# Kernel tuning notes

Measured on AMD Instinct MI355X. Metric: run time of the kernel, lower is better.

Reference implementation:

```python
import jax, jax.numpy as jnp
import numpy as np
from jax import lax

B, T, NX, NY = 4, 5, 512, 512
HID = 64
N_FP = 4
INV_R = 1000.0


def _build_Q():
    # 7-point space-time Laplacian stencil on the (t, y, x) grid, matching
    # torch.permute(x[i], (0, 2, 1)).flatten() ordering (t outer, y, x inner).
    idx = np.arange(T * NY * NX, dtype=np.int32).reshape(T, NY, NX)
    rows = [idx.ravel()]
    cols = [idx.ravel()]
    vals = [np.full(idx.size, 6.01, np.float32)]  # diag: 6 neighbors + kappa^2

    def add(a, b):
        rows.append(a.ravel()); cols.append(b.ravel())
        vals.append(np.full(a.size, -1.0, np.float32))
        rows.append(b.ravel()); cols.append(a.ravel())
        vals.append(np.full(a.size, -1.0, np.float32))

    add(idx[:-1], idx[1:])          # t neighbors
    add(idx[:, :-1], idx[:, 1:])    # y neighbors
    add(idx[:, :, :-1], idx[:, :, 1:])  # x neighbors
    return (np.concatenate(rows), np.concatenate(cols), np.concatenate(vals))


def setup_inputs() -> dict:
    key = jax.random.key(0)
    ks = jax.random.split(key, 7)
    gt = jax.random.normal(ks[0], (B, T, NX, NY), jnp.float32)
    x = jax.random.normal(ks[1], (B, T, NX, NY), jnp.float32)
    yobs = jax.random.normal(ks[2], (B, T, NX, NY), jnp.float32)
    mask = jax.random.randint(ks[3], (B, T, NX, NY), 0, 2).astype(jnp.int32)
    W1 = jax.random.normal(ks[4], (HID, T, 3, 3), jnp.float32) * 0.05
    b1 = jnp.zeros((HID,), jnp.float32)
    W2 = jax.random.normal(ks[5], (T, HID, 3, 3), jnp.float32) * 0.05
    b2 = jnp.zeros((T,), jnp.float32)
    qr, qc, qv = _build_Q()
    return {"gt": gt, "x": x, "yobs": yobs, "mask": mask,
            "W1": W1, "b1": b1, "W2": W2, "b2": b2,
            "Q_rows": jnp.asarray(qr), "Q_cols": jnp.asarray(qc),
            "Q_vals": jnp.asarray(qv), "n_fp": N_FP}


def _phi_r(x, W1, b1, W2, b2):
    dn = ("NCHW", "OIHW", "NCHW")
    h = lax.conv_general_dilated(x, W1, (1, 1), "SAME", dimension_numbers=dn)
    h = jax.nn.relu(h + b1[None, :, None, None])
    o = lax.conv_general_dilated(h, W2, (1, 1), "SAME", dimension_numbers=dn)
    return o + b2[None, :, None, None]


def _var_cost_row(gt, x, yobs, maskf, Q_rows, Q_cols, Q_vals):
    # dy term: inv_R = 1000*I restricted to observed entries
    dy = (x - yobs) * maskf                       # model_H
    dy_term = INV_R * jnp.sum(maskf * dy * dy, axis=(1, 2, 3))  # [B]
    # x^T Q x on the permuted/flattened field (sparse COO quadratic form)
    xp = jnp.transpose(x, (0, 1, 3, 2)).reshape(x.shape[0], -1)  # [B, T*NY*NX]
    xtQx = jnp.einsum("bn,n,bn->b", xp[:, Q_rows], Q_vals, xp[:, Q_cols])
    loss_OI = dy_term + xtQx
    # weighted MSE with w = ones(5) == plain per-batch MSE
    loss_mse = jnp.mean((gt - x) ** 2, axis=(1, 2, 3))
    return jnp.stack([loss_mse, loss_OI], axis=1)  # [B, 2]


def reference(gt, x, yobs, mask, W1, b1, W2, b2, Q_rows, Q_cols, Q_vals, n_fp):
    maskf = mask.astype(x.dtype)
    unmeas = 1.0 - maskf
    y_obs = yobs * maskf
    x_k = x
    rows = []
    for _ in range(n_fp):
        rows.append(_var_cost_row(gt, x_k, yobs, maskf, Q_rows, Q_cols, Q_vals))
        x_k = _phi_r(x_k, W1, b1, W2, b2) * unmeas + y_obs  # fixed-point step
    x_k = _phi_r(x_k, W1, b1, W2, b2)
    rows.append(_var_cost_row(gt, x_k, yobs, maskf, Q_rows, Q_cols, Q_vals))
    cmp_loss = jnp.stack(rows, axis=1)  # [B, n_fp+1, 2]
    return x_k, cmp_loss
```

## Files before the change

kernel.cpp:

```cpp
#include <hip/hip_runtime.h>
#include <hip/hip_bf16.h>

#define NXD 512
#define NYD 512
#define TD 5
#define BD 4
#define HIDD 64
#define PLANE (NXD*NYD)
#define VOL (TD*PLANE)
#define CBLK 1024

typedef __bf16 bf16x8 __attribute__((ext_vector_type(8)));
typedef __bf16 bf16x4 __attribute__((ext_vector_type(4)));
typedef float  f32x4  __attribute__((ext_vector_type(4)));

#define SX_PS 16
#define SH_PS 80

#define W1R_ELEMS (3*64*32)
#define W2R_ELEMS (2*9*16*32)

__global__ __launch_bounds__(256)
void prep_weights(const float* __restrict__ W1, const float* __restrict__ W2,
                  __bf16* __restrict__ W1r, __bf16* __restrict__ W2r)
{
    int id = blockIdx.x * 256 + threadIdx.x;
    if (id < W1R_ELEMS) {
        int kt  = id >> 11;
        int rem = id & 2047;
        int n   = rem >> 5;
        int kk  = rem & 31;
        int k   = kt * 32 + kk;
        int tap = k >> 3, c = k & 7;
        float v = 0.f;
        if (tap <= 8 && c < 5)
            v = W1[(n * 5 + c) * 9 + tap];
        W1r[id] = (__bf16)v;
    } else if (id < W1R_ELEMS + W2R_ELEMS) {
        int id2 = id - W1R_ELEMS;
        int h    = id2 / 4608;
        int rem  = id2 - h * 4608;
        int tap  = rem >> 9;
        int rem2 = rem & 511;
        int n    = rem2 >> 5;
        int c    = rem2 & 31;
        float v = 0.f;
        if (n < 5)
            v = W2[(n * HIDD + h * 32 + c) * 9 + tap];
        W2r[id2] = (__bf16)v;
    }
}

template<int INP, int OUTP>
__global__ __launch_bounds__(256, 4)
void phi_mfma(const float* __restrict__ xin,
              const __bf16* __restrict__ xin_pk,
              const __bf16* __restrict__ W1r, const __bf16* __restrict__ W2r,
              const float* __restrict__ b1, const float* __restrict__ b2,
              const float* __restrict__ gt, const float* __restrict__ yobs,
              const int* __restrict__ mask,
              float* __restrict__ xout, __bf16* __restrict__ xout_pk,
              float* __restrict__ cpart, int blend)
{
    __shared__ __align__(16) char sx[400 * SX_PS];
    __shared__ __align__(16) char sh[324 * SH_PS];

    const int tid   = threadIdx.x;
    const int wv    = tid >> 6;
    const int lane  = tid & 63;
    const int l15   = lane & 15;
    const int quad  = lane >> 4;
    const int b     = blockIdx.z;
    const int gx0   = blockIdx.x * 16;
    const int gy0   = blockIdx.y * 16;

    for (int p = tid; p < 400; p += 256) {
        const int u  = p / 20;
        const int v  = p - u * 20;
        const int gx = gx0 + u - 2;
        const int gy = gy0 + v - 2;
        bf16x8 pix = {(__bf16)0.f,(__bf16)0.f,(__bf16)0.f,(__bf16)0.f,
                      (__bf16)0.f,(__bf16)0.f,(__bf16)0.f,(__bf16)0.f};
        if (gx >= 0 && gx < NXD && gy >= 0 && gy < NYD) {
            if constexpr (INP == 0) {
                const float* src = xin + (size_t)b * VOL + (size_t)gx * NYD + gy;
                #pragma unroll
                for (int c = 0; c < TD; ++c) pix[c] = (__bf16)src[(size_t)c * PLANE];
            } else {
                pix = *(const bf16x8*)(xin_pk +
                        ((size_t)b * PLANE + (size_t)gx * NYD + gy) * 8);
            }
        }
        *(bf16x8*)(sx + p * SX_PS) = pix;
    }
    __syncthreads();

    if (cpart) {
        const int ti = tid >> 4, tj = tid & 15;
        const int u  = ti + 2,  v  = tj + 2;
        const size_t gbase = (size_t)b * VOL + (size_t)(gx0 + ti) * NYD + (gy0 + tj);
        float xv[TD];
        if constexpr (INP == 0) {
            #pragma unroll
            for (int c = 0; c < TD; ++c) xv[c] = xin[gbase + (size_t)c * PLANE];
        } else {
            bf16x8 pxv = *(const bf16x8*)(xin_pk +
                ((size_t)b * PLANE + (size_t)(gx0 + ti) * NYD + (gy0 + tj)) * 8);
            #pragma unroll
            for (int c = 0; c < TD; ++c) xv[c] = (float)pxv[c];
        }
        float mse = 0.f, dy = 0.f, q = 0.f;
        #pragma unroll
        for (int c = 0; c < TD; ++c) {
            const size_t gi = gbase + (size_t)c * PLANE;
            const float vv = xv[c];
            const float g  = gt[gi];
            const float yo = yobs[gi];
            const int   m  = mask[gi];
            mse += (g - vv) * (g - vv);
            float d = vv - yo;
            if (m) dy += d * d;
            float xp1 = (float)*(const __bf16*)(sx + (u * 20 + v + 1) * SX_PS + c * 2);
            float yp1 = (float)*(const __bf16*)(sx + ((u + 1) * 20 + v) * SX_PS + c * 2);
            float tp1 = (c < TD - 1)
                      ? (float)*(const __bf16*)(sx + (u * 20 + v) * SX_PS + (c + 1) * 2)
                      : 0.f;
            q += 6.01f * vv * vv - 2.f * vv * (xp1 + yp1 + tp1);
        }
        #pragma unroll
        for (int off = 32; off > 0; off >>= 1) {
            mse += __shfl_xor(mse, off, 64);
            dy  += __shfl_xor(dy,  off, 64);
            q   += __shfl_xor(q,   off, 64);
        }
        if (lane == 0) {
            float* pp = cpart + (((size_t)b * 1024 + blockIdx.y * 32 + blockIdx.x) * 4 + wv) * 3;
            pp[0] = mse; pp[1] = dy; pp[2] = q;
        }
    }

    f32x4 acc2[4] = {{0.f,0.f,0.f,0.f},{0.f,0.f,0.f,0.f},
                     {0.f,0.f,0.f,0.f},{0.f,0.f,0.f,0.f}};

    for (int half = 0; half < 2; ++half) {
        bf16x8 A1[2][3];
        f32x4  bias1[2];
        #pragma unroll
        for (int mt = 0; mt < 2; ++mt) {
            bias1[mt] = *(const f32x4*)(b1 + half * 32 + mt * 16 + quad * 4);
            #pragma unroll
            for (int kt = 0; kt < 3; ++kt)
                A1[mt][kt] = *(const bf16x8*)(W1r +
                    ((size_t)(kt * 64 + half * 32 + mt * 16 + l15) * 32 + quad * 8));
        }
        if (half) __syncthreads();

        #pragma unroll 2
        for (int nt = 0; nt < 6; ++nt) {
            const int ntg = wv * 6 + nt;
            const int p   = ntg * 16 + l15;
            const int pc  = (p < 324) ? p : 323;
            const int i   = pc / 18;
            const int j   = pc - 18 * i;
            const int pb  = (i * 20 + j) * SX_PS;
            bf16x8 Bx[3];
            #pragma unroll
            for (int kt = 0; kt < 3; ++kt) {
                int tap = kt * 4 + quad;
                if (tap > 8) tap = 8;
                Bx[kt] = *(const bf16x8*)(sx + pb + ((tap / 3) * 20 + tap % 3) * SX_PS);
            }
            #pragma unroll
            for (int mt = 0; mt < 2; ++mt) {
                f32x4 a = {0.f, 0.f, 0.f, 0.f};
                #pragma unroll
                for (int kt = 0; kt < 3; ++kt)
                    a = __builtin_amdgcn_mfma_f32_16x16x32_bf16(
                            A1[mt][kt], Bx[kt], a, 0, 0, 0);
                if (p < 324) {
                    bf16x4 hv;
                    #pragma unroll
                    for (int r = 0; r < 4; ++r)
                        hv[r] = (__bf16)fmaxf(a[r] + bias1[mt][r], 0.f);
                    *(bf16x4*)(sh + p * SH_PS + (mt * 16 + quad * 4) * 2) = hv;
                }
            }
        }
        __syncthreads();

        bf16x8 A2[9];
        #pragma unroll
        for (int tap = 0; tap < 9; ++tap)
            A2[tap] = *(const bf16x8*)(W2r +
                ((size_t)((half * 9 + tap) * 16 + l15) * 32 + quad * 8));

        const int shbase = (wv * 4 * 18 + l15) * SH_PS + quad * 16;
        bf16x8 R[6][3];
        #pragma unroll
        for (int rr = 0; rr < 3; ++rr)
            #pragma unroll
            for (int tx = 0; tx < 3; ++tx)
                R[rr][tx] = *(const bf16x8*)(sh + shbase + (rr * 18 + tx) * SH_PS);
        #pragma unroll
        for (int m = 0; m < 4; ++m) {
            #pragma unroll
            for (int dy = 0; dy < 3; ++dy)
                #pragma unroll
                for (int tx = 0; tx < 3; ++tx)
                    acc2[m] = __builtin_amdgcn_mfma_f32_16x16x32_bf16(
                                  A2[dy * 3 + tx], R[m + dy][tx], acc2[m], 0, 0, 0);
            if (m < 3) {
                #pragma unroll
                for (int tx = 0; tx < 3; ++tx)
                    R[m + 3][tx] = *(const bf16x8*)(sh + shbase +
                                                    ((m + 3) * 18 + tx) * SH_PS);
            }
        }
    }

    float b2v[4];
    #pragma unroll
    for (int r = 0; r < 4; ++r) {
        const int ch = quad * 4 + r;
        b2v[r] = (ch < TD) ? b2[ch] : 0.f;
    }
    if constexpr (OUTP == 0) {
        #pragma unroll
        for (int m = 0; m < 4; ++m) {
            const int ti2 = wv * 4 + m;
            const size_t rowoff = (size_t)b * VOL + (size_t)(gx0 + ti2) * NYD + (gy0 + l15);
            #pragma unroll
            for (int r = 0; r < 4; ++r) {
                const int ch = quad * 4 + r;
                if (ch < TD) {
                    const size_t off = rowoff + (size_t)ch * PLANE;
                    float o = acc2[m][r] + b2v[r];
                    if (blend && mask[off]) o = yobs[off];
                    xout[off] = o;
                }
            }
        }
    } else {
        const float b2_4 = b2[4];
        #pragma unroll
        for (int m = 0; m < 4; ++m) {
            const int ti2 = wv * 4 + m;
            const float c4 = __shfl(acc2[m][0], 16 + l15, 64) + b2_4;
            if (quad == 0) {
                const size_t poff = (size_t)b * VOL +
                                    (size_t)(gx0 + ti2) * NYD + (gy0 + l15);
                float o[TD];
                #pragma unroll
                for (int r = 0; r < 4; ++r) o[r] = acc2[m][r] + b2v[r];
                o[4] = c4;
                if (blend) {
                    #pragma unroll
                    for (int ch = 0; ch < TD; ++ch) {
                        const size_t off = poff + (size_t)ch * PLANE;
                        if (mask[off]) o[ch] = yobs[off];
                    }
                }
                bf16x8 pk = {(__bf16)o[0], (__bf16)o[1], (__bf16)o[2],
                             (__bf16)o[3], (__bf16)o[4],
                             (__bf16)0.f, (__bf16)0.f, (__bf16)0.f};
                *(bf16x8*)(xout_pk + ((size_t)b * PLANE +
                    (size_t)(gx0 + ti2) * NYD + (gy0 + l15)) * 8) = pk;
            }
        }
    }
}

__global__ __launch_bounds__(256)
void cost_kernel(const float* __restrict__ x, const float* __restrict__ gt,
                 const float* __restrict__ yobs, const int* __restrict__ mask,
                 float* __restrict__ partial)
{
    const int b  = blockIdx.y;
    const size_t bbase = (size_t)b * VOL;

    float mse = 0.f, dy = 0.f, q = 0.f;
    for (int idx = blockIdx.x * 256 + threadIdx.x; idx < VOL; idx += CBLK * 256) {
        const size_t gi = bbase + idx;
        const int t   = idx / PLANE;
        const int rem = idx - t * PLANE;
        const int i   = rem / NYD;
        const int j   = rem - i * NYD;

        const float v  = x[gi];
        const float g  = gt[gi];
        const float yo = yobs[gi];
        const int   m  = mask[gi];

        mse += (g - v) * (g - v);
        float d = v - yo;
        if (m) dy += d * d;
        float qq = 6.01f * v * v;
        if (t < TD - 1)  qq -= 2.f * v * x[gi + PLANE];
        if (i < NXD - 1) qq -= 2.f * v * x[gi + NYD];
        if (j < NYD - 1) qq -= 2.f * v * x[gi + 1];
        q += qq;
    }

    #pragma unroll
    for (int off = 32; off > 0; off >>= 1) {
        mse += __shfl_xor(mse, off, 64);
        dy  += __shfl_xor(dy,  off, 64);
        q   += __shfl_xor(q,   off, 64);
    }
    const int wave = threadIdx.x >> 6;
    const int lane = threadIdx.x & 63;
    if (lane == 0) {
        float* p = partial + (((size_t)b * CBLK + blockIdx.x) * 4 + wave) * 3;
        p[0] = mse; p[1] = dy; p[2] = q;
    }
}

__global__ __launch_bounds__(256)
void finalize_kernel(const float* __restrict__ cpart,
                     float* __restrict__ out)
{
    const int r = blockIdx.x / BD;
    const int b = blockIdx.x - r * BD;
    const float* base = cpart + ((size_t)r * BD + b) * 4096 * 3;
    float mse = 0.f, dy = 0.f, q = 0.f;
    for (int k = threadIdx.x; k < 4096; k += 256) {
        mse += base[k * 3 + 0];
        dy  += base[k * 3 + 1];
        q   += base[k * 3 + 2];
    }
    #pragma unroll
    for (int off = 32; off > 0; off >>= 1) {
        mse += __shfl_xor(mse, off, 64);
        dy  += __shfl_xor(dy,  off, 64);
        q   += __shfl_xor(q,   off, 64);
    }
    __shared__ float red[3][4];
    const int wave = threadIdx.x >> 6;
    const int lane = threadIdx.x & 63;
    if (lane == 0) { red[0][wave] = mse; red[1][wave] = dy; red[2][wave] = q; }
    __syncthreads();
    if (threadIdx.x == 0) {
        float m  = red[0][0] + red[0][1] + red[0][2] + red[0][3];
        float d  = red[1][0] + red[1][1] + red[1][2] + red[1][3];
        float qq = red[2][0] + red[2][1] + red[2][2] + red[2][3];
        out[b * 10 + r * 2 + 0] = m / (float)VOL;
        out[b * 10 + r * 2 + 1] = 1000.f * d + qq;
    }
}

extern "C" void kernel_launch(void* const* d_in, const int* in_sizes, int n_in,
                              void* d_out, int out_size, void* d_ws, size_t ws_size,
                              hipStream_t stream)
{
    const float* gt   = (const float*)d_in[0];
    const float* x0   = (const float*)d_in[1];
    const float* yobs = (const float*)d_in[2];
    const int*   mask = (const int*)d_in[3];
    const float* W1   = (const float*)d_in[4];
    const float* b1   = (const float*)d_in[5];
    const float* W2   = (const float*)d_in[6];
    const float* b2   = (const float*)d_in[7];

    float* out_x    = (float*)d_out;
    float* out_loss = out_x + (size_t)BD * VOL;

    float* wsA      = (float*)d_ws;
    float* cpart    = wsA + (size_t)BD * VOL;
    __bf16* W1r     = (__bf16*)(cpart + 5 * BD * 4096 * 3);
    __bf16* W2r     = W1r + W1R_ELEMS;
    const size_t PROW = (size_t)BD * 4096 * 3;

    __bf16* Pout = (__bf16*)out_x;
    __bf16* Pws  = (__bf16*)wsA;

    dim3 pgrid(NXD / 16, NYD / 16, BD), pblock(256);
    dim3 cgrid(CBLK, BD), cblock(256);

    prep_weights<<<dim3(60), dim3(256), 0, stream>>>(W1, W2, W1r, W2r);

    phi_mfma<0,1><<<pgrid, pblock, 0, stream>>>(x0, nullptr, W1r, W2r, b1, b2,
        gt, yobs, mask, nullptr, Pout, cpart + 0 * PROW, 1);
    phi_mfma<1,1><<<pgrid, pblock, 0, stream>>>(nullptr, Pout, W1r, W2r, b1, b2,
        gt, yobs, mask, nullptr, Pws,  cpart + 1 * PROW, 1);
    phi_mfma<1,1><<<pgrid, pblock, 0, stream>>>(nullptr, Pws,  W1r, W2r, b1, b2,
        gt, yobs, mask, nullptr, Pout, cpart + 2 * PROW, 1);
    phi_mfma<1,1><<<pgrid, pblock, 0, stream>>>(nullptr, Pout, W1r, W2r, b1, b2,
        gt, yobs, mask, nullptr, Pws,  cpart + 3 * PROW, 1);
    phi_mfma<1,0><<<pgrid, pblock, 0, stream>>>(nullptr, Pws,  W1r, W2r, b1, b2,
        gt, yobs, mask, out_x, nullptr, nullptr, 0);
    cost_kernel<<<cgrid, cblock, 0, stream>>>(out_x, gt, yobs, mask, cpart + 4 * PROW);

    finalize_kernel<<<dim3(5 * BD), dim3(256), 0, stream>>>(cpart, out_loss);
}
```

Baseline: 543.7 us.

## Widen phi tile to 16x32 pixels, processing two column subtiles per block

Each phi block now loads a 20x36 halo tile into shared memory and runs the two-layer conv over two 16-column subtiles in sequence, so the halo overhead per output pixel drops and the grid halves. The cost partials, the cost kernel grid and the finalize reduction are resized to 512 partial blocks per batch. The trade-off is more shared memory per block, which may lower occupancy, half as many blocks to spread over the CUs, and an extra barrier between subtiles.

```diff
diff --git a/kernel.cpp b/kernel.cpp
--- a/kernel.cpp
+++ b/kernel.cpp
@@ -8,13 +8,14 @@
 #define HIDD 64
 #define PLANE (NXD*NYD)
 #define VOL (TD*PLANE)
-#define CBLK 1024
+#define NPB 512
 
 typedef __bf16 bf16x8 __attribute__((ext_vector_type(8)));
 typedef __bf16 bf16x4 __attribute__((ext_vector_type(4)));
 typedef float  f32x4  __attribute__((ext_vector_type(4)));
 
 #define SX_PS 16
+#define SXW 36
 #define SH_PS 80
 
 #define W1R_ELEMS (3*64*32)
@@ -62,7 +63,7 @@
               float* __restrict__ xout, __bf16* __restrict__ xout_pk,
               float* __restrict__ cpart, int blend)
 {
-    __shared__ __align__(16) char sx[400 * SX_PS];
+    __shared__ __align__(16) char sx[720 * SX_PS];
     __shared__ __align__(16) char sh[324 * SH_PS];
 
     const int tid   = threadIdx.x;
@@ -72,11 +73,11 @@
     const int quad  = lane >> 4;
     const int b     = blockIdx.z;
     const int gx0   = blockIdx.x * 16;
-    const int gy0   = blockIdx.y * 16;
-
-    for (int p = tid; p < 400; p += 256) {
-        const int u  = p / 20;
-        const int v  = p - u * 20;
+    const int gy0   = blockIdx.y * 32;
+
+    for (int p = tid; p < 720; p += 256) {
+        const int u  = p / SXW;
+        const int v  = p - u * SXW;
         const int gx = gx0 + u - 2;
         const int gy = gy0 + v - 2;
         bf16x8 pix = {(__bf16)0.f,(__bf16)0.f,(__bf16)0.f,(__bf16)0.f,
@@ -97,35 +98,38 @@
 
     if (cpart) {
         const int ti = tid >> 4, tj = tid & 15;
-        const int u  = ti + 2,  v  = tj + 2;
-        const size_t gbase = (size_t)b * VOL + (size_t)(gx0 + ti) * NYD + (gy0 + tj);
-        float xv[TD];
-        if constexpr (INP == 0) {
-            #pragma unroll
-            for (int c = 0; c < TD; ++c) xv[c] = xin[gbase + (size_t)c * PLANE];
-        } else {
-            bf16x8 pxv = *(const bf16x8*)(xin_pk +
-                ((size_t)b * PLANE + (size_t)(gx0 + ti) * NYD + (gy0 + tj)) * 8);
-            #pragma unroll
-            for (int c = 0; c < TD; ++c) xv[c] = (float)pxv[c];
-        }
         float mse = 0.f, dy = 0.f, q = 0.f;
-        #pragma unroll
-        for (int c = 0; c < TD; ++c) {
-            const size_t gi = gbase + (size_t)c * PLANE;
-            const float vv = xv[c];
-            const float g  = gt[gi];
-            const float yo = yobs[gi];
-            const int   m  = mask[gi];
-            mse += (g - vv) * (g - vv);
-            float d = vv - yo;
-            if (m) dy += d * d;
-            float xp1 = (float)*(const __bf16*)(sx + (u * 20 + v + 1) * SX_PS + c * 2);
-            float yp1 = (float)*(const __bf16*)(sx + ((u + 1) * 20 + v) * SX_PS + c * 2);
-            float tp1 = (c < TD - 1)
-                      ? (float)*(const __bf16*)(sx + (u * 20 + v) * SX_PS + (c + 1) * 2)
-                      : 0.f;
-            q += 6.01f * vv * vv - 2.f * vv * (xp1 + yp1 + tp1);
+        for (int ct = 0; ct < 2; ++ct) {
+            const int col = ct * 16 + tj;
+            const int u   = ti + 2, v = col + 2;
+            const size_t gbase = (size_t)b * VOL + (size_t)(gx0 + ti) * NYD + (gy0 + col);
+            float xv[TD];
+            if constexpr (INP == 0) {
+                #pragma unroll
+                for (int c = 0; c < TD; ++c) xv[c] = xin[gbase + (size_t)c * PLANE];
+            } else {
+                bf16x8 pxv = *(const bf16x8*)(xin_pk +
+                    ((size_t)b * PLANE + (size_t)(gx0 + ti) * NYD + (gy0 + col)) * 8);
+                #pragma unroll
+                for (int c = 0; c < TD; ++c) xv[c] = (float)pxv[c];
+            }
+            #pragma unroll
+            for (int c = 0; c < TD; ++c) {
+                const size_t gi = gbase + (size_t)c * PLANE;
+                const float vv = xv[c];
+                const float g  = gt[gi];
+                const float yo = yobs[gi];
+                const int   m  = mask[gi];
+                mse += (g - vv) * (g - vv);
+                float d = vv - yo;
+                if (m) dy += d * d;
+                float xp1 = (float)*(const __bf16*)(sx + (u * SXW + v + 1) * SX_PS + c * 2);
+                float yp1 = (float)*(const __bf16*)(sx + ((u + 1) * SXW + v) * SX_PS + c * 2);
+                float tp1 = (c < TD - 1)
+                          ? (float)*(const __bf16*)(sx + (u * SXW + v) * SX_PS + (c + 1) * 2)
+                          : 0.f;
+                q += 6.01f * vv * vv - 2.f * vv * (xp1 + yp1 + tp1);
+            }
         }
         #pragma unroll
         for (int off = 32; off > 0; off >>= 1) {
@@ -134,137 +138,142 @@
             q   += __shfl_xor(q,   off, 64);
         }
         if (lane == 0) {
-            float* pp = cpart + (((size_t)b * 1024 + blockIdx.y * 32 + blockIdx.x) * 4 + wv) * 3;
+            const int tile = blockIdx.y * 32 + blockIdx.x;
+            float* pp = cpart + (((size_t)b * NPB + tile) * 4 + wv) * 3;
             pp[0] = mse; pp[1] = dy; pp[2] = q;
         }
     }
 
-    f32x4 acc2[4] = {{0.f,0.f,0.f,0.f},{0.f,0.f,0.f,0.f},
-                     {0.f,0.f,0.f,0.f},{0.f,0.f,0.f,0.f}};
-
-    for (int half = 0; half < 2; ++half) {
-        bf16x8 A1[2][3];
-        f32x4  bias1[2];
-        #pragma unroll
-        for (int mt = 0; mt < 2; ++mt) {
-            bias1[mt] = *(const f32x4*)(b1 + half * 32 + mt * 16 + quad * 4);
-            #pragma unroll
-            for (int kt = 0; kt < 3; ++kt)
-                A1[mt][kt] = *(const bf16x8*)(W1r +
-                    ((size_t)(kt * 64 + half * 32 + mt * 16 + l15) * 32 + quad * 8));
-        }
-        if (half) __syncthreads();
-
-        #pragma unroll 2
-        for (int nt = 0; nt < 6; ++nt) {
-            const int ntg = wv * 6 + nt;
-            const int p   = ntg * 16 + l15;
-            const int pc  = (p < 324) ? p : 323;
-            const int i   = pc / 18;
-            const int j   = pc - 18 * i;
-            const int pb  = (i * 20 + j) * SX_PS;
-            bf16x8 Bx[3];
-            #pragma unroll
-            for (int kt = 0; kt < 3; ++kt) {
-                int tap = kt * 4 + quad;
-                if (tap > 8) tap = 8;
-                Bx[kt] = *(const bf16x8*)(sx + pb + ((tap / 3) * 20 + tap % 3) * SX_PS);
-            }
+    for (int ct = 0; ct < 2; ++ct) {
+        f32x4 acc2[4] = {{0.f,0.f,0.f,0.f},{0.f,0.f,0.f,0.f},
+                         {0.f,0.f,0.f,0.f},{0.f,0.f,0.f,0.f}};
+
+        for (int half = 0; half < 2; ++half) {
+            bf16x8 A1[2][3];
+            f32x4  bias1[2];
             #pragma unroll
             for (int mt = 0; mt < 2; ++mt) {
-                f32x4 a = {0.f, 0.f, 0.f, 0.f};
+                bias1[mt] = *(const f32x4*)(b1 + half * 32 + mt * 16 + quad * 4);
                 #pragma unroll
                 for (int kt = 0; kt < 3; ++kt)
-                    a = __builtin_amdgcn_mfma_f32_16x16x32_bf16(
-                            A1[mt][kt], Bx[kt], a, 0, 0, 0);
-                if (p < 324) {
-                    bf16x4 hv;
+                    A1[mt][kt] = *(const bf16x8*)(W1r +
+                        ((size_t)(kt * 64 + half * 32 + mt * 16 + l15) * 32 + quad * 8));
+            }
+            if (ct || half) __syncthreads();
+
+            #pragma unroll 2
+            for (int nt = 0; nt < 6; ++nt) {
+                const int ntg = wv * 6 + nt;
+                const int p   = ntg * 16 + l15;
+                const int pc  = (p < 324) ? p : 323;
+                const int i   = pc / 18;
+                const int j   = pc - 18 * i;
+                const int pb  = (i * SXW + j + ct * 16) * SX_PS;
+                bf16x8 Bx[3];
+                #pragma unroll
+                for (int kt = 0; kt < 3; ++kt) {
+                    int tap = kt * 4 + quad;
+                    if (tap > 8) tap = 8;
+                    Bx[kt] = *(const bf16x8*)(sx + pb +
+                              ((tap / 3) * SXW + tap % 3) * SX_PS);
+                }
+                #pragma unroll
+                for (int mt = 0; mt < 2; ++mt) {
+                    f32x4 a = {0.f, 0.f, 0.f, 0.f};
                     #pragma unroll
-                    for (int r = 0; r < 4; ++r)
-                        hv[r] = (__bf16)fmaxf(a[r] + bias1[mt][r], 0.f);
-                    *(bf16x4*)(sh + p * SH_PS + (mt * 16 + quad * 4) * 2) = hv;
-                }
-            }
-        }
-        __syncthreads();
-
-        bf16x8 A2[9];
-        #pragma unroll
-        for (int tap = 0; tap < 9; ++tap)
-            A2[tap] = *(const bf16x8*)(W2r +
-                ((size_t)((half * 9 + tap) * 16 + l15) * 32 + quad * 8));
-
-        const int shbase = (wv * 4 * 18 + l15) * SH_PS + quad * 16;
-        bf16x8 R[6][3];
-        #pragma unroll
-        for (int rr = 0; rr < 3; ++rr)
-            #pragma unroll
-            for (int tx = 0; tx < 3; ++tx)
-                R[rr][tx] = *(const bf16x8*)(sh + shbase + (rr * 18 + tx) * SH_PS);
-        #pragma unroll
-        for (int m = 0; m < 4; ++m) {
-            #pragma unroll
-            for (int dy = 0; dy < 3; ++dy)
-                #pragma unroll
-                for (int tx = 0; tx < 3; ++tx)
-                    acc2[m] = __builtin_amdgcn_mfma_f32_16x16x32_bf16(
-                                  A2[dy * 3 + tx], R[m + dy][tx], acc2[m], 0, 0, 0);
-            if (m < 3) {
-                #pragma unroll
-                for (int tx = 0; tx < 3; ++tx)
-                    R[m + 3][tx] = *(const bf16x8*)(sh + shbase +
-                                                    ((m + 3) * 18 + tx) * SH_PS);
-            }
-        }
-    }
-
-    float b2v[4];
-    #pragma unroll
-    for (int r = 0; r < 4; ++r) {
-        const int ch = quad * 4 + r;
-        b2v[r] = (ch < TD) ? b2[ch] : 0.f;
-    }
-    if constexpr (OUTP == 0) {
-        #pragma unroll
-        for (int m = 0; m < 4; ++m) {
-            const int ti2 = wv * 4 + m;
-            const size_t rowoff = (size_t)b * VOL + (size_t)(gx0 + ti2) * NYD + (gy0 + l15);
-            #pragma unroll
-            for (int r = 0; r < 4; ++r) {
-                const int ch = quad * 4 + r;
-                if (ch < TD) {
-                    const size_t off = rowoff + (size_t)ch * PLANE;
-                    float o = acc2[m][r] + b2v[r];
-                    if (blend && mask[off]) o = yobs[off];
-                    xout[off] = o;
-                }
-            }
-        }
-    } else {
-        const float b2_4 = b2[4];
-        #pragma unroll
-        for (int m = 0; m < 4; ++m) {
-            const int ti2 = wv * 4 + m;
-            const float c4 = __shfl(acc2[m][0], 16 + l15, 64) + b2_4;
-            if (quad == 0) {
-                const size_t poff = (size_t)b * VOL +
-                                    (size_t)(gx0 + ti2) * NYD + (gy0 + l15);
-                float o[TD];
-                #pragma unroll
-                for (int r = 0; r < 4; ++r) o[r] = acc2[m][r] + b2v[r];
-                o[4] = c4;
-                if (blend) {
-                    #pragma unroll
-                    for (int ch = 0; ch < TD; ++ch) {
-                        const size_t off = poff + (size_t)ch * PLANE;
-                        if (mask[off]) o[ch] = yobs[off];
+                    for (int kt = 0; kt < 3; ++kt)
+                        a = __builtin_amdgcn_mfma_f32_16x16x32_bf16(
+                                A1[mt][kt], Bx[kt], a, 0, 0, 0);
+                    if (p < 324) {
+                        bf16x4 hv;
+                        #pragma unroll
+                        for (int r = 0; r < 4; ++r)
+                            hv[r] = (__bf16)fmaxf(a[r] + bias1[mt][r], 0.f);
+                        *(bf16x4*)(sh + p * SH_PS + (mt * 16 + quad * 4) * 2) = hv;
                     }
                 }
-                bf16x8 pk = {(__bf16)o[0], (__bf16)o[1], (__bf16)o[2],
-                             (__bf16)o[3], (__bf16)o[4],
-                             (__bf16)0.f, (__bf16)0.f, (__bf16)0.f};
-                *(bf16x8*)(xout_pk + ((size_t)b * PLANE +
-                    (size_t)(gx0 + ti2) * NYD + (gy0 + l15)) * 8) = pk;
+            }
+            __syncthreads();
+
+            bf16x8 A2[9];
+            #pragma unroll
+            for (int tap = 0; tap < 9; ++tap)
+                A2[tap] = *(const bf16x8*)(W2r +
+                    ((size_t)((half * 9 + tap) * 16 + l15) * 32 + quad * 8));
+
+            const int shbase = (wv * 4 * 18 + l15) * SH_PS + quad * 16;
+            bf16x8 R[6][3];
+            #pragma unroll
+            for (int rr = 0; rr < 3; ++rr)
+                #pragma unroll
+                for (int tx = 0; tx < 3; ++tx)
+                    R[rr][tx] = *(const bf16x8*)(sh + shbase + (rr * 18 + tx) * SH_PS);
+            #pragma unroll
+            for (int m = 0; m < 4; ++m) {
+                #pragma unroll
+                for (int dy = 0; dy < 3; ++dy)
+                    #pragma unroll
+                    for (int tx = 0; tx < 3; ++tx)
+                        acc2[m] = __builtin_amdgcn_mfma_f32_16x16x32_bf16(
+                                      A2[dy * 3 + tx], R[m + dy][tx], acc2[m], 0, 0, 0);
+                if (m < 3) {
+                    #pragma unroll
+                    for (int tx = 0; tx < 3; ++tx)
+                        R[m + 3][tx] = *(const bf16x8*)(sh + shbase +
+                                                        ((m + 3) * 18 + tx) * SH_PS);
+                }
+            }
+        }
+
+        float b2v[4];
+        #pragma unroll
+        for (int r = 0; r < 4; ++r) {
+            const int ch = quad * 4 + r;
+            b2v[r] = (ch < TD) ? b2[ch] : 0.f;
+        }
+        if constexpr (OUTP == 0) {
+            #pragma unroll
+            for (int m = 0; m < 4; ++m) {
+                const int ti2 = wv * 4 + m;
+                const size_t rowoff = (size_t)b * VOL +
+                    (size_t)(gx0 + ti2) * NYD + (gy0 + ct * 16 + l15);
+                #pragma unroll
+                for (int r = 0; r < 4; ++r) {
+                    const int ch = quad * 4 + r;
+                    if (ch < TD) {
+                        const size_t off = rowoff + (size_t)ch * PLANE;
+                        float o = acc2[m][r] + b2v[r];
+                        if (blend && mask[off]) o = yobs[off];
+                        xout[off] = o;
+                    }
+                }
+            }
+        } else {
+            const float b2_4 = b2[4];
+            #pragma unroll
+            for (int m = 0; m < 4; ++m) {
+                const int ti2 = wv * 4 + m;
+                const float c4 = __shfl(acc2[m][0], 16 + l15, 64) + b2_4;
+                if (quad == 0) {
+                    const size_t poff = (size_t)b * VOL +
+                        (size_t)(gx0 + ti2) * NYD + (gy0 + ct * 16 + l15);
+                    float o[TD];
+                    #pragma unroll
+                    for (int r = 0; r < 4; ++r) o[r] = acc2[m][r] + b2v[r];
+                    o[4] = c4;
+                    if (blend) {
+                        #pragma unroll
+                        for (int ch = 0; ch < TD; ++ch) {
+                            const size_t off = poff + (size_t)ch * PLANE;
+                            if (mask[off]) o[ch] = yobs[off];
+                        }
+                    }
+                    bf16x8 pk = {(__bf16)o[0], (__bf16)o[1], (__bf16)o[2],
+                                 (__bf16)o[3], (__bf16)o[4],
+                                 (__bf16)0.f, (__bf16)0.f, (__bf16)0.f};
+                    *(bf16x8*)(xout_pk + ((size_t)b * PLANE +
+                        (size_t)(gx0 + ti2) * NYD + (gy0 + ct * 16 + l15)) * 8) = pk;
+                }
             }
         }
     }
@@ -279,7 +288,7 @@
     const size_t bbase = (size_t)b * VOL;
 
     float mse = 0.f, dy = 0.f, q = 0.f;
-    for (int idx = blockIdx.x * 256 + threadIdx.x; idx < VOL; idx += CBLK * 256) {
+    for (int idx = blockIdx.x * 256 + threadIdx.x; idx < VOL; idx += NPB * 256) {
         const size_t gi = bbase + idx;
         const int t   = idx / PLANE;
         const int rem = idx - t * PLANE;
@@ -310,7 +319,7 @@
     const int wave = threadIdx.x >> 6;
     const int lane = threadIdx.x & 63;
     if (lane == 0) {
-        float* p = partial + (((size_t)b * CBLK + blockIdx.x) * 4 + wave) * 3;
+        float* p = partial + (((size_t)b * NPB + blockIdx.x) * 4 + wave) * 3;
         p[0] = mse; p[1] = dy; p[2] = q;
     }
 }
@@ -321,9 +330,9 @@
 {
     const int r = blockIdx.x / BD;
     const int b = blockIdx.x - r * BD;
-    const float* base = cpart + ((size_t)r * BD + b) * 4096 * 3;
+    const float* base = cpart + ((size_t)r * BD + b) * (NPB * 4) * 3;
     float mse = 0.f, dy = 0.f, q = 0.f;
-    for (int k = threadIdx.x; k < 4096; k += 256) {
+    for (int k = threadIdx.x; k < NPB * 4; k += 256) {
         mse += base[k * 3 + 0];
         dy  += base[k * 3 + 1];
         q   += base[k * 3 + 2];
@@ -366,15 +375,15 @@
 
     float* wsA      = (float*)d_ws;
     float* cpart    = wsA + (size_t)BD * VOL;
-    __bf16* W1r     = (__bf16*)(cpart + 5 * BD * 4096 * 3);
+    __bf16* W1r     = (__bf16*)(cpart + 5 * BD * (NPB * 4) * 3);
     __bf16* W2r     = W1r + W1R_ELEMS;
-    const size_t PROW = (size_t)BD * 4096 * 3;
+    const size_t PROW = (size_t)BD * (NPB * 4) * 3;
 
     __bf16* Pout = (__bf16*)out_x;
     __bf16* Pws  = (__bf16*)wsA;
 
-    dim3 pgrid(NXD / 16, NYD / 16, BD), pblock(256);
-    dim3 cgrid(CBLK, BD), cblock(256);
+    dim3 pgrid(NXD / 16, NYD / 32, BD), pblock(256);
+    dim3 cgrid(NPB, BD), cblock(256);
 
     prep_weights<<<dim3(60), dim3(256), 0, stream>>>(W1, W2, W1r, W2r);
 
```

Result: slower. 707.0 us (+30.0%).
